# Performance work log

Measured on AMD Instinct MI355X. Metric: run time of the kernel, lower is better.

The kernel has to match this reference:

```python
import jax, jax.numpy as jnp
import numpy as np

HIDDEN = 512
HEADS = 8
HEAD_DIM = HIDDEN // HEADS
EPS_LN = 1e-5
EPS_ATTN = 1e-6


def setup_inputs() -> dict:
    key = jax.random.key(0)
    ks = jax.random.split(key, 12)
    B, S, N, D = 4, 12, 2048, HIDDEN
    s = 1.0 / np.sqrt(D)
    x = jax.random.normal(ks[0], (B, S, N, D), dtype=jnp.float32)
    Wq = jax.random.normal(ks[1], (D, D), dtype=jnp.float32) * s
    bq = jnp.zeros((D,), dtype=jnp.float32)
    Wk = jax.random.normal(ks[2], (D, D), dtype=jnp.float32) * s
    bk = jnp.zeros((D,), dtype=jnp.float32)
    Wv = jax.random.normal(ks[3], (D, D), dtype=jnp.float32) * s
    bv = jnp.zeros((D,), dtype=jnp.float32)
    Wo = jax.random.normal(ks[4], (D, D), dtype=jnp.float32) * s
    bo = jnp.zeros((D,), dtype=jnp.float32)
    ln_g = jnp.ones((D,), dtype=jnp.float32)
    ln_b = jnp.zeros((D,), dtype=jnp.float32)
    return {"x": x, "Wq": Wq, "bq": bq, "Wk": Wk, "bk": bk,
            "Wv": Wv, "bv": bv, "Wo": Wo, "bo": bo,
            "ln_g": ln_g, "ln_b": ln_b}


def _layer_norm(x, g, b):
    mu = jnp.mean(x, axis=-1, keepdims=True)
    var = jnp.var(x, axis=-1, keepdims=True)
    return (x - mu) * jax.lax.rsqrt(var + EPS_LN) * g + b


def reference(x, Wq, bq, Wk, bk, Wv, bv, Wo, bo, ln_g, ln_b):
    B, S, N, D = x.shape
    L = S * N  # flattened spatiotemporal tokens
    residual = x
    h = _layer_norm(x, ln_g, ln_b).reshape(B, L, D)
    # projections; [B, L, D] -> [B, H, L, hd]
    def split_heads(t):
        return t.reshape(B, L, HEADS, HEAD_DIM).transpose(0, 2, 1, 3)
    q = split_heads(h @ Wq.T + bq)
    k = split_heads(h @ Wk.T + bk)
    v = split_heads(h @ Wv.T + bv)
    # elu+1 feature map
    q = jax.nn.elu(q) + 1.0
    k = jax.nn.elu(k) + 1.0
    # kv outer product: [B, H, hd, hd]
    kv = jnp.einsum('bhld,bhle->bhde', k, v)
    out = jnp.einsum('bhld,bhde->bhle', q, kv)
    normalizer = jnp.einsum('bhld,bhd->bhl', q, k.sum(axis=2))
    out = out / (normalizer[..., None] + EPS_ATTN)
    out = out.transpose(0, 2, 1, 3).reshape(B, L, D)
    out = out @ Wo.T + bo
    out = out.reshape(B, S, N, D)
    return out + residual
```

## Files before the change

### kernel.cpp

```cpp
#include <hip/hip_runtime.h>
#include <hip/hip_bf16.h>
#include <stdint.h>

#define DDIM 512
#define NHEAD 8
#define BATCH 4
#define LTOK 24576
#define MROWS 98304
#define MBLK 768
#define MBLK_B 192
#define PTILE 4160

typedef __attribute__((ext_vector_type(8))) short short8;
typedef __attribute__((ext_vector_type(4))) float f32x4;

__device__ __forceinline__ float bf2f(unsigned short u) {
  union { unsigned int i; float f; } c; c.i = ((unsigned int)u) << 16; return c.f;
}
__device__ __forceinline__ unsigned short f2bf(float f) {
  union { float f; unsigned int i; } c; c.f = f;
  unsigned int r = c.i + 0x7FFFu + ((c.i >> 16) & 1u);
  return (unsigned short)(r >> 16);
}
__device__ __forceinline__ void gload16(const void* g, void* l) {
  __builtin_amdgcn_global_load_lds((const __attribute__((address_space(1))) void*)g,
                                   (__attribute__((address_space(3))) void*)l, 16, 0, 0);
}
__device__ __forceinline__ float elu1(float v) { return (v > 0.f) ? (v + 1.f) : __expf(v); }

__global__ __launch_bounds__(256) void wprep(const float* __restrict__ Wq, const float* __restrict__ bq,
                                             const float* __restrict__ Wk, const float* __restrict__ bk,
                                             const float* __restrict__ Wv, const float* __restrict__ bv,
                                             const float* __restrict__ Wo,
                                             unsigned short* __restrict__ wf,
                                             unsigned short* __restrict__ wob,
                                             float* __restrict__ biasf) {
  long t = (long)blockIdx.x * 256 + threadIdx.x;
  if (t < 786432) {
    int f = (int)(t >> 9), c = (int)(t & 511);
    const float* src;
    if (f < 1024) { int hh = f >> 7, kv = (f >> 6) & 1, d = f & 63;
                    src = (kv ? Wv : Wk) + (long)(hh * 64 + d) * 512; }
    else          src = Wq + (long)(f - 1024) * 512;
    wf[t] = f2bf(src[c]);
  } else if (t < 786432 + 262144) {
    long i = t - 786432; wob[i] = f2bf(Wo[i]);
  } else if (t < 786432 + 262144 + 1536) {
    int f = (int)(t - (786432 + 262144));
    float v;
    if (f < 1024) { int hh = f >> 7, kv = (f >> 6) & 1, d = f & 63; v = (kv ? bv : bk)[hh * 64 + d]; }
    else v = bq[f - 1024];
    biasf[f] = v;
  }
}

__global__ __launch_bounds__(256) void ln_kernel(const float* __restrict__ x,
                                                 const float* __restrict__ g,
                                                 const float* __restrict__ b,
                                                 unsigned short* __restrict__ h) {
  int wv = threadIdx.x >> 6, lane = threadIdx.x & 63;
  long row = (long)blockIdx.x * 4 + wv;
  const float* xr = x + row * DDIM + lane * 8;
  float4 v0 = *(const float4*)xr;
  float4 v1 = *(const float4*)(xr + 4);
  float s  = v0.x + v0.y + v0.z + v0.w + v1.x + v1.y + v1.z + v1.w;
  float s2 = v0.x*v0.x + v0.y*v0.y + v0.z*v0.z + v0.w*v0.w
           + v1.x*v1.x + v1.y*v1.y + v1.z*v1.z + v1.w*v1.w;
  #pragma unroll
  for (int o = 32; o; o >>= 1) { s += __shfl_xor(s, o); s2 += __shfl_xor(s2, o); }
  float mu = s * (1.0f / DDIM);
  float var = s2 * (1.0f / DDIM) - mu * mu;
  float rs = rsqrtf(var + 1e-5f);
  float4 g0 = *(const float4*)(g + lane * 8);
  float4 g1 = *(const float4*)(g + lane * 8 + 4);
  float4 b0 = *(const float4*)(b + lane * 8);
  float4 b1 = *(const float4*)(b + lane * 8 + 4);
  short8 o;
  o[0] = (short)f2bf((v0.x - mu) * rs * g0.x + b0.x);
  o[1] = (short)f2bf((v0.y - mu) * rs * g0.y + b0.y);
  o[2] = (short)f2bf((v0.z - mu) * rs * g0.z + b0.z);
  o[3] = (short)f2bf((v0.w - mu) * rs * g0.w + b0.w);
  o[4] = (short)f2bf((v1.x - mu) * rs * g1.x + b1.x);
  o[5] = (short)f2bf((v1.y - mu) * rs * g1.y + b1.y);
  o[6] = (short)f2bf((v1.z - mu) * rs * g1.z + b1.z);
  o[7] = (short)f2bf((v1.w - mu) * rs * g1.w + b1.w);
  *(short8*)(h + row * DDIM + lane * 8) = o;
}

__global__ __launch_bounds__(256) void qkv_gemm(const unsigned short* __restrict__ A,
                                                const unsigned short* __restrict__ wf,
                                                const float* __restrict__ biasf,
                                                unsigned short* __restrict__ qbuf,
                                                unsigned short* __restrict__ part) {
  __shared__ union {
    struct { unsigned short As[128 * 64]; unsigned short Bs[128 * 64]; } st;
    struct { unsigned short kT[64 * 136]; unsigned short vT[64 * 136]; } tr;
    unsigned short Cs[128 * 136];
  } sm;

  int t = threadIdx.x;
  int wv = t >> 6, lane = t & 63;
  int wm = wv >> 1, wn = wv & 1;
  int kg = lane >> 4, lr = lane & 15;

  int lin = blockIdx.x;
  int g = lin / 96, r = lin % 96;
  int xb = g * 8 + (r & 7);
  int y  = r >> 3;
  long mBase = (long)xb * 128;
  int nBase = y * 128;

  f32x4 acc[4][4];
  #pragma unroll
  for (int m = 0; m < 4; m++)
    #pragma unroll
    for (int n = 0; n < 4; n++) acc[m][n] = (f32x4){0.f, 0.f, 0.f, 0.f};

  const unsigned short* Ab = A + mBase * DDIM;
  const unsigned short* Wb = wf + (long)nBase * DDIM;

  for (int k0 = 0; k0 < DDIM; k0 += 64) {
    #pragma unroll
    for (int i = 0; i < 4; i++) {
      int c = i * 256 + t;
      int rr = c >> 3, cc = c & 7;
      int sc = ((cc ^ (rr & 7)) << 3);
      gload16(Ab + (long)rr * DDIM + k0 + sc, sm.st.As + c * 8);
      gload16(Wb + (long)rr * DDIM + k0 + sc, sm.st.Bs + c * 8);
    }
    __syncthreads();
    #pragma unroll
    for (int kk = 0; kk < 2; kk++) {
      short8 a[4], b[4];
      #pragma unroll
      for (int m = 0; m < 4; m++) {
        int row = wm * 64 + m * 16 + lr;
        a[m] = *(const short8*)&sm.st.As[row * 64 + (((kk * 4 + kg) ^ (row & 7)) << 3)];
      }
      #pragma unroll
      for (int n = 0; n < 4; n++) {
        int row = wn * 64 + n * 16 + lr;
        b[n] = *(const short8*)&sm.st.Bs[row * 64 + (((kk * 4 + kg) ^ (row & 7)) << 3)];
      }
      #pragma unroll
      for (int m = 0; m < 4; m++)
        #pragma unroll
        for (int n = 0; n < 4; n++)
          acc[m][n] = __builtin_amdgcn_mfma_f32_16x16x32_bf16(a[m], b[n], acc[m][n], 0, 0, 0);
    }
    __syncthreads();
  }

  if (y < 8) {
    #pragma unroll
    for (int n = 0; n < 4; n++) {
      int col = wn * 64 + n * 16 + lr;
      float bv = biasf[nBase + col];
      #pragma unroll
      for (int m = 0; m < 4; m++)
        #pragma unroll
        for (int j = 0; j < 4; j++) {
          int row = wm * 64 + m * 16 + kg * 4 + j;
          float v = acc[m][n][j] + bv;
          if (wn == 0) sm.tr.kT[col * 136 + row] = f2bf(elu1(v));
          else         sm.tr.vT[(col - 64) * 136 + row] = f2bf(v);
        }
    }
    __syncthreads();
    f32x4 pacc[4];
    #pragma unroll
    for (int n = 0; n < 4; n++) pacc[n] = (f32x4){0.f, 0.f, 0.f, 0.f};
    short8 a[4];
    #pragma unroll
    for (int kk = 0; kk < 4; kk++)
      a[kk] = *(const short8*)&sm.tr.kT[(wv * 16 + lr) * 136 + kk * 32 + kg * 8];
    #pragma unroll
    for (int n = 0; n < 4; n++)
      #pragma unroll
      for (int kk = 0; kk < 4; kk++) {
        short8 b = *(const short8*)&sm.tr.vT[(n * 16 + lr) * 136 + kk * 32 + kg * 8];
        pacc[n] = __builtin_amdgcn_mfma_f32_16x16x32_bf16(a[kk], b, pacc[n], 0, 0, 0);
      }
    int batch = (int)(mBase / LTOK);
    int cIdx = xb % MBLK_B;
    long pbase = ((long)(batch * 8 + y) * MBLK_B + cIdx) * PTILE;
    #pragma unroll
    for (int n = 0; n < 4; n++)
      #pragma unroll
      for (int j = 0; j < 4; j++) {
        int d = wv * 16 + kg * 4 + j, e = n * 16 + lr;
        part[pbase + d * 64 + e] = f2bf(pacc[n][j]);
      }
    if (t < 64) {
      float s = 0.f;
      #pragma unroll
      for (int p = 0; p < 16; p++) {
        short8 kk8 = *(const short8*)&sm.tr.kT[t * 136 + p * 8];
        #pragma unroll
        for (int q = 0; q < 8; q++) s += bf2f((unsigned short)kk8[q]);
      }
      part[pbase + 4096 + t] = f2bf(s);
    }
  } else {
    #pragma unroll
    for (int n = 0; n < 4; n++) {
      int col = wn * 64 + n * 16 + lr;
      float bv = biasf[nBase + col];
      #pragma unroll
      for (int m = 0; m < 4; m++)
        #pragma unroll
        for (int j = 0; j < 4; j++) {
          int row = wm * 64 + m * 16 + kg * 4 + j;
          sm.Cs[row * 136 + col] = f2bf(elu1(acc[m][n][j] + bv));
        }
    }
    __syncthreads();
    int nq = y - 8;
    #pragma unroll
    for (int p = 0; p < 8; p++) {
      int idx = p * 256 + t;
      int row = idx >> 4, c8 = idx & 15;
      *(short8*)&qbuf[(mBase + row) * DDIM + nq * 128 + c8 * 8] =
          *(const short8*)&sm.Cs[row * 136 + c8 * 8];
    }
  }
}

__global__ __launch_bounds__(256) void kv_final(const unsigned short* __restrict__ part,
                                                unsigned short* __restrict__ kvD,
                                                float* __restrict__ ksum) {
  int bh = blockIdx.x;
  int idx = blockIdx.y * 256 + threadIdx.x;
  if (idx >= PTILE) return;
  const unsigned short* base = part + (long)bh * MBLK_B * PTILE + idx;
  float s = 0.f;
  for (int c = 0; c < MBLK_B; c++) s += bf2f(base[(long)c * PTILE]);
  if (idx < 4096) kvD[bh * 4096 + idx] = f2bf(s);
  else            ksum[bh * 64 + (idx - 4096)] = s;
}

__global__ __launch_bounds__(512) void w2_gemm(const unsigned short* __restrict__ kvD,
                                               const unsigned short* __restrict__ wob,
                                               unsigned short* __restrict__ Bmat) {
  __shared__ unsigned short W2s[512 * 72];
  int t = threadIdx.x, wv = t >> 6, lane = t & 63;
  int kg = lane >> 4, lr = lane & 15;
  int bh = blockIdx.x, b = bh >> 3, h = bh & 7;
  const unsigned short* kva = kvD + bh * 4096;

  short8 a[4][2];
  #pragma unroll
  for (int m = 0; m < 4; m++)
    #pragma unroll
    for (int kk = 0; kk < 2; kk++)
      a[m][kk] = *(const short8*)&kva[(m * 16 + lr) * 64 + kk * 32 + kg * 8];

  f32x4 acc[4][4];
  #pragma unroll
  for (int m = 0; m < 4; m++)
    #pragma unroll
    for (int n = 0; n < 4; n++) acc[m][n] = (f32x4){0.f, 0.f, 0.f, 0.f};

  #pragma unroll
  for (int n = 0; n < 4; n++) {
    int c = wv * 64 + n * 16 + lr;
    #pragma unroll
    for (int kk = 0; kk < 2; kk++) {
      short8 bfr = *(const short8*)&wob[(long)c * 512 + h * 64 + kk * 32 + kg * 8];
      #pragma unroll
      for (int m = 0; m < 4; m++)
        acc[m][n] = __builtin_amdgcn_mfma_f32_16x16x32_bf16(a[m][kk], bfr, acc[m][n], 0, 0, 0);
    }
  }
  #pragma unroll
  for (int m = 0; m < 4; m++)
    #pragma unroll
    for (int n = 0; n < 4; n++)
      #pragma unroll
      for (int j = 0; j < 4; j++)
        W2s[(wv * 64 + n * 16 + lr) * 72 + m * 16 + kg * 4 + j] = f2bf(acc[m][n][j]);
  __syncthreads();
  #pragma unroll
  for (int pp = 0; pp < 8; pp++) {
    int idx = pp * 512 + t;
    int c = idx >> 3, ch = (idx & 7) * 8;
    *(short8*)&Bmat[(long)b * 262144 + (long)c * 512 + h * 64 + ch] =
        *(const short8*)&W2s[c * 72 + ch];
  }
}

__global__ __launch_bounds__(256) void qscale(unsigned short* __restrict__ q,
                                              const float* __restrict__ ksum) {
  int wv = threadIdx.x >> 6, lane = threadIdx.x & 63;
  long row = (long)blockIdx.x * 4 + wv;
  int batch = (int)(row / LTOK);
  int bh = batch * 8 + (lane >> 3);
  unsigned short* qr = q + row * DDIM + lane * 8;
  short8 qv = *(const short8*)qr;
  const float* ks = ksum + bh * 64 + (lane & 7) * 8;
  float4 k0 = *(const float4*)ks;
  float4 k1 = *(const float4*)(ks + 4);
  float qf[8];
  #pragma unroll
  for (int j = 0; j < 8; j++) qf[j] = bf2f((unsigned short)qv[j]);
  float n = qf[0]*k0.x + qf[1]*k0.y + qf[2]*k0.z + qf[3]*k0.w
          + qf[4]*k1.x + qf[5]*k1.y + qf[6]*k1.z + qf[7]*k1.w;
  n += __shfl_xor(n, 1);
  n += __shfl_xor(n, 2);
  n += __shfl_xor(n, 4);
  float s = 1.0f / (n + 1e-6f);
  short8 o;
  #pragma unroll
  for (int j = 0; j < 8; j++) o[j] = (short)f2bf(qf[j] * s);
  *(short8*)qr = o;
}

__global__ __launch_bounds__(256) void ogemm(const unsigned short* __restrict__ A,
                                             const unsigned short* __restrict__ Bm,
                                             const float* __restrict__ bo,
                                             const float* __restrict__ xres,
                                             float* __restrict__ out) {
  __shared__ union {
    struct { unsigned short As[128 * 64]; unsigned short Bs[128 * 64]; } st;
    float Cs[64 * 132];
  } sm;

  int t = threadIdx.x;
  int wv = t >> 6, lane = t & 63;
  int wm = wv >> 1, wn = wv & 1;
  int kg = lane >> 4, lr = lane & 15;

  int lin = blockIdx.x;
  int g = lin >> 5, r = lin & 31;
  int xb = g * 8 + (r & 7);
  int y  = r >> 3;
  long mBase = (long)xb * 128;
  int nBase = y * 128;
  int batch = xb / MBLK_B;

  f32x4 acc[4][4];
  #pragma unroll
  for (int m = 0; m < 4; m++)
    #pragma unroll
    for (int n = 0; n < 4; n++) acc[m][n] = (f32x4){0.f, 0.f, 0.f, 0.f};

  const unsigned short* Ab = A + mBase * DDIM;
  const unsigned short* Bb = Bm + (long)batch * 262144 + (long)nBase * DDIM;

  for (int k0 = 0; k0 < DDIM; k0 += 64) {
    #pragma unroll
    for (int i = 0; i < 4; i++) {
      int c = i * 256 + t;
      int rr = c >> 3, cc = c & 7;
      int sc = ((cc ^ (rr & 7)) << 3);
      gload16(Ab + (long)rr * DDIM + k0 + sc, sm.st.As + c * 8);
      gload16(Bb + (long)rr * DDIM + k0 + sc, sm.st.Bs + c * 8);
    }
    __syncthreads();
    #pragma unroll
    for (int kk = 0; kk < 2; kk++) {
      short8 a[4], b[4];
      #pragma unroll
      for (int m = 0; m < 4; m++) {
        int row = wm * 64 + m * 16 + lr;
        a[m] = *(const short8*)&sm.st.As[row * 64 + (((kk * 4 + kg) ^ (row & 7)) << 3)];
      }
      #pragma unroll
      for (int n = 0; n < 4; n++) {
        int row = wn * 64 + n * 16 + lr;
        b[n] = *(const short8*)&sm.st.Bs[row * 64 + (((kk * 4 + kg) ^ (row & 7)) << 3)];
      }
      #pragma unroll
      for (int m = 0; m < 4; m++)
        #pragma unroll
        for (int n = 0; n < 4; n++)
          acc[m][n] = __builtin_amdgcn_mfma_f32_16x16x32_bf16(a[m], b[n], acc[m][n], 0, 0, 0);
    }
    __syncthreads();
  }

  for (int p = 0; p < 2; p++) {
    __syncthreads();
    if (wm == p) {
      #pragma unroll
      for (int n = 0; n < 4; n++) {
        int col = wn * 64 + n * 16 + lr;
        float bv = bo[nBase + col];
        #pragma unroll
        for (int m = 0; m < 4; m++)
          #pragma unroll
          for (int j = 0; j < 4; j++) {
            int lrow = m * 16 + kg * 4 + j;
            sm.Cs[lrow * 132 + col] = acc[m][n][j] + bv;
          }
      }
    }
    __syncthreads();
    #pragma unroll
    for (int pp = 0; pp < 8; pp++) {
      int idx = pp * 256 + t;
      int row = idx >> 5, c4 = idx & 31;
      long goff = (mBase + p * 64 + row) * DDIM + nBase + c4 * 4;
      float4 rv = *(const float4*)&xres[goff];
      float4 cv = *(const float4*)&sm.Cs[row * 132 + c4 * 4];
      float4 ov; ov.x = cv.x + rv.x; ov.y = cv.y + rv.y; ov.z = cv.z + rv.z; ov.w = cv.w + rv.w;
      *(float4*)&out[goff] = ov;
    }
  }
}

extern "C" void kernel_launch(void* const* d_in, const int* in_sizes, int n_in,
                              void* d_out, int out_size, void* d_ws, size_t ws_size,
                              hipStream_t stream) {
  const float* x    = (const float*)d_in[0];
  const float* Wq   = (const float*)d_in[1];
  const float* bq   = (const float*)d_in[2];
  const float* Wk   = (const float*)d_in[3];
  const float* bk   = (const float*)d_in[4];
  const float* Wv   = (const float*)d_in[5];
  const float* bv   = (const float*)d_in[6];
  const float* Wo   = (const float*)d_in[7];
  const float* bo   = (const float*)d_in[8];
  const float* ln_g = (const float*)d_in[9];
  const float* ln_b = (const float*)d_in[10];

  char* ws = (char*)d_ws;
  size_t SZ = (size_t)MROWS * DDIM * 2;
  unsigned short* hbuf = (unsigned short*)ws;
  unsigned short* qbuf = (unsigned short*)(ws + SZ);
  char* p = ws + 2 * SZ;
  unsigned short* wf   = (unsigned short*)p;  p += (size_t)1536 * 512 * 2;
  unsigned short* wob  = (unsigned short*)p;  p += (size_t)512 * 512 * 2;
  float* biasf         = (float*)p;           p += 1536 * 4;
  p = (char*)(((uintptr_t)p + 255) & ~(uintptr_t)255);
  unsigned short* part = (unsigned short*)p;  p += (size_t)6144 * PTILE * 2;
  unsigned short* kvD  = (unsigned short*)p;  p += (size_t)32 * 4096 * 2;
  float* ksum          = (float*)p;           p += 32 * 64 * 4;
  p = (char*)(((uintptr_t)p + 255) & ~(uintptr_t)255);
  unsigned short* Bmat = (unsigned short*)p;  p += (size_t)BATCH * 512 * 512 * 2;

  wprep<<<(786432 + 262144 + 1536 + 255) / 256, 256, 0, stream>>>(Wq, bq, Wk, bk, Wv, bv, Wo,
                                                                  wf, wob, biasf);
  ln_kernel<<<MROWS / 4, 256, 0, stream>>>(x, ln_g, ln_b, hbuf);
  qkv_gemm<<<MBLK * 12, 256, 0, stream>>>(hbuf, wf, biasf, qbuf, part);
  kv_final<<<dim3(32, (PTILE + 255) / 256), 256, 0, stream>>>(part, kvD, ksum);
  w2_gemm<<<32, 512, 0, stream>>>(kvD, wob, Bmat);
  qscale<<<MROWS / 4, 256, 0, stream>>>(qbuf, ksum);
  ogemm<<<MBLK * 4, 256, 0, stream>>>(qbuf, Bmat, bo, x, (float*)d_out);
}
```

Measured before the change: 511.4 us.

## Rewrite QKV GEMM with 256x256 tiles and a double-buffered pipelined K loop

The QKV projection GEMM moves from 128x128 tiles with 256 threads to 256x256 tiles with 512 threads. The K loop is restructured into half-tile stages over a 128KB LDS double buffer, with explicit vmcnt waits, s_setprio and sched barriers so global-to-LDS loads overlap the MFMA work. The KV partial epilogue now handles two heads per block and gets the key sum from an MFMA against a ones row, which halves the partial buffer and the kv_final reduction depth. The cost is higher register and LDS pressure, much larger unrolled code, and hand-counted waitcnt values that must stay correct.

```diff
diff --git a/kernel.cpp b/kernel.cpp
--- a/kernel.cpp
+++ b/kernel.cpp
@@ -7,8 +7,10 @@
 #define BATCH 4
 #define LTOK 24576
 #define MROWS 98304
-#define MBLK 768
-#define MBLK_B 192
+#define QKV_MBLK 384
+#define KVCH 96
+#define OG_MBLK 768
+#define OG_MBLK_B 192
 #define PTILE 4160
 
 typedef __attribute__((ext_vector_type(8))) short short8;
@@ -87,141 +89,251 @@
   *(short8*)(h + row * DDIM + lane * 8) = o;
 }
 
-__global__ __launch_bounds__(256) void qkv_gemm(const unsigned short* __restrict__ A,
-                                                const unsigned short* __restrict__ wf,
-                                                const float* __restrict__ biasf,
-                                                unsigned short* __restrict__ qbuf,
-                                                unsigned short* __restrict__ part) {
-  __shared__ union {
-    struct { unsigned short As[128 * 64]; unsigned short Bs[128 * 64]; } st;
-    struct { unsigned short kT[64 * 136]; unsigned short vT[64 * 136]; } tr;
-    unsigned short Cs[128 * 136];
-  } sm;
-
-  int t = threadIdx.x;
-  int wv = t >> 6, lane = t & 63;
-  int wm = wv >> 1, wn = wv & 1;
+
+__device__ __forceinline__ short8 ldsfrag(const unsigned short* h, int row, int kg) {
+  return *(const short8*)&h[row * 32 + ((kg ^ ((row >> 1) & 3)) << 3)];
+}
+
+__device__ __forceinline__ void stage_half(const unsigned short* gbase,
+                                           unsigned short* ldsbase, int tid) {
+  #pragma unroll
+  for (int i = 0; i < 2; i++) {
+    int c = i * 512 + tid;
+    int rr = c >> 2, cc = c & 3;
+    int sc = ((cc ^ ((rr >> 1) & 3)) << 3);
+    gload16(gbase + (long)rr * DDIM + sc, ldsbase + c * 8);
+  }
+}
+
+template <int VMP1, int VMP3, bool S01, bool S23>
+__device__ __forceinline__ void ktile(int t, unsigned short* lds,
+                                      const unsigned short* Ab, const unsigned short* Wb,
+                                      f32x4 (&acc)[8][4],
+                                      int wm, int wn, int lr, int kg, int tid) {
+  const int buf = t & 1;
+  unsigned short* A0l = lds + (buf * 2 + 0) * 8192;
+  unsigned short* A1l = lds + (buf * 2 + 1) * 8192;
+  unsigned short* B0l = lds + 32768 + (buf * 2 + 0) * 8192;
+  unsigned short* B1l = lds + 32768 + (buf * 2 + 1) * 8192;
+  unsigned short* A1n = lds + ((buf ^ 1) * 2 + 1) * 8192;
+  unsigned short* B1n = lds + 32768 + ((buf ^ 1) * 2 + 1) * 8192;
+  short8 a[4], b[4];
+
+  #pragma unroll
+  for (int m = 0; m < 4; m++) a[m] = ldsfrag(A0l, wm * 128 + m * 16 + lr, kg);
+  #pragma unroll
+  for (int n = 0; n < 4; n++) b[n] = ldsfrag(B0l, wn * 64 + n * 16 + lr, kg);
+  if (S01) stage_half(Ab + (long)(t + 1) * 64 + 32, A1n, tid);
+  __builtin_amdgcn_s_barrier();
+  __builtin_amdgcn_s_setprio(1);
+  #pragma unroll
+  for (int m = 0; m < 4; m++)
+    #pragma unroll
+    for (int n = 0; n < 4; n++)
+      acc[m][n] = __builtin_amdgcn_mfma_f32_16x16x32_bf16(a[m], b[n], acc[m][n], 0, 0, 0);
+  __builtin_amdgcn_s_setprio(0);
+  __builtin_amdgcn_s_barrier();
+  __builtin_amdgcn_sched_barrier(0);
+
+  #pragma unroll
+  for (int m = 0; m < 4; m++) a[m] = ldsfrag(A0l, wm * 128 + (4 + m) * 16 + lr, kg);
+  if (S01) stage_half(Wb + (long)(t + 1) * 64 + 32, B1n, tid);
+  __builtin_amdgcn_s_barrier();
+  __builtin_amdgcn_s_setprio(1);
+  #pragma unroll
+  for (int m = 0; m < 4; m++)
+    #pragma unroll
+    for (int n = 0; n < 4; n++)
+      acc[4 + m][n] = __builtin_amdgcn_mfma_f32_16x16x32_bf16(a[m], b[n], acc[4 + m][n], 0, 0, 0);
+  __builtin_amdgcn_s_setprio(0);
+  asm volatile("s_waitcnt vmcnt(%0)" :: "i"(VMP1) : "memory");
+  __builtin_amdgcn_s_barrier();
+  __builtin_amdgcn_sched_barrier(0);
+
+  #pragma unroll
+  for (int m = 0; m < 4; m++) a[m] = ldsfrag(A1l, wm * 128 + m * 16 + lr, kg);
+  #pragma unroll
+  for (int n = 0; n < 4; n++) b[n] = ldsfrag(B1l, wn * 64 + n * 16 + lr, kg);
+  if (S23) stage_half(Ab + (long)(t + 2) * 64, A0l, tid);
+  __builtin_amdgcn_s_barrier();
+  __builtin_amdgcn_s_setprio(1);
+  #pragma unroll
+  for (int m = 0; m < 4; m++)
+    #pragma unroll
+    for (int n = 0; n < 4; n++)
+      acc[m][n] = __builtin_amdgcn_mfma_f32_16x16x32_bf16(a[m], b[n], acc[m][n], 0, 0, 0);
+  __builtin_amdgcn_s_setprio(0);
+  __builtin_amdgcn_s_barrier();
+  __builtin_amdgcn_sched_barrier(0);
+
+  #pragma unroll
+  for (int m = 0; m < 4; m++) a[m] = ldsfrag(A1l, wm * 128 + (4 + m) * 16 + lr, kg);
+  if (S23) stage_half(Wb + (long)(t + 2) * 64, B0l, tid);
+  __builtin_amdgcn_s_barrier();
+  __builtin_amdgcn_s_setprio(1);
+  #pragma unroll
+  for (int m = 0; m < 4; m++)
+    #pragma unroll
+    for (int n = 0; n < 4; n++)
+      acc[4 + m][n] = __builtin_amdgcn_mfma_f32_16x16x32_bf16(a[m], b[n], acc[4 + m][n], 0, 0, 0);
+  __builtin_amdgcn_s_setprio(0);
+  asm volatile("s_waitcnt vmcnt(%0)" :: "i"(VMP3) : "memory");
+  __builtin_amdgcn_s_barrier();
+  __builtin_amdgcn_sched_barrier(0);
+}
+
+__global__ __launch_bounds__(512, 2) void qkv_gemm(const unsigned short* __restrict__ A,
+                                                   const unsigned short* __restrict__ wf,
+                                                   const float* __restrict__ biasf,
+                                                   unsigned short* __restrict__ qbuf,
+                                                   unsigned short* __restrict__ part) {
+  __shared__ unsigned short lds[65536];
+
+  int tid = threadIdx.x;
+  int wv = tid >> 6, lane = tid & 63;
+  int wm = wv >> 2, wn = wv & 3;
   int kg = lane >> 4, lr = lane & 15;
 
   int lin = blockIdx.x;
-  int g = lin / 96, r = lin % 96;
+  int g = lin / 48, r = lin % 48;
   int xb = g * 8 + (r & 7);
   int y  = r >> 3;
-  long mBase = (long)xb * 128;
-  int nBase = y * 128;
-
-  f32x4 acc[4][4];
-  #pragma unroll
-  for (int m = 0; m < 4; m++)
-    #pragma unroll
-    for (int n = 0; n < 4; n++) acc[m][n] = (f32x4){0.f, 0.f, 0.f, 0.f};
+  long mBase = (long)xb * 256;
+  int nBase = y * 256;
 
   const unsigned short* Ab = A + mBase * DDIM;
   const unsigned short* Wb = wf + (long)nBase * DDIM;
 
-  for (int k0 = 0; k0 < DDIM; k0 += 64) {
-    #pragma unroll
-    for (int i = 0; i < 4; i++) {
-      int c = i * 256 + t;
-      int rr = c >> 3, cc = c & 7;
-      int sc = ((cc ^ (rr & 7)) << 3);
-      gload16(Ab + (long)rr * DDIM + k0 + sc, sm.st.As + c * 8);
-      gload16(Wb + (long)rr * DDIM + k0 + sc, sm.st.Bs + c * 8);
-    }
-    __syncthreads();
-    #pragma unroll
-    for (int kk = 0; kk < 2; kk++) {
-      short8 a[4], b[4];
-      #pragma unroll
-      for (int m = 0; m < 4; m++) {
-        int row = wm * 64 + m * 16 + lr;
-        a[m] = *(const short8*)&sm.st.As[row * 64 + (((kk * 4 + kg) ^ (row & 7)) << 3)];
-      }
-      #pragma unroll
-      for (int n = 0; n < 4; n++) {
-        int row = wn * 64 + n * 16 + lr;
-        b[n] = *(const short8*)&sm.st.Bs[row * 64 + (((kk * 4 + kg) ^ (row & 7)) << 3)];
-      }
-      #pragma unroll
-      for (int m = 0; m < 4; m++)
-        #pragma unroll
-        for (int n = 0; n < 4; n++)
-          acc[m][n] = __builtin_amdgcn_mfma_f32_16x16x32_bf16(a[m], b[n], acc[m][n], 0, 0, 0);
-    }
-    __syncthreads();
-  }
-
-  if (y < 8) {
-    #pragma unroll
-    for (int n = 0; n < 4; n++) {
-      int col = wn * 64 + n * 16 + lr;
-      float bv = biasf[nBase + col];
-      #pragma unroll
-      for (int m = 0; m < 4; m++)
+  f32x4 acc[8][4];
+  #pragma unroll
+  for (int m = 0; m < 8; m++)
+    #pragma unroll
+    for (int n = 0; n < 4; n++) acc[m][n] = (f32x4){0.f, 0.f, 0.f, 0.f};
+
+  stage_half(Ab,       lds + 0 * 8192, tid);
+  stage_half(Wb,       lds + 32768 + 0 * 8192, tid);
+  stage_half(Ab + 32,  lds + 1 * 8192, tid);
+  stage_half(Wb + 32,  lds + 32768 + 1 * 8192, tid);
+  stage_half(Ab + 64,  lds + 2 * 8192, tid);
+  stage_half(Wb + 64,  lds + 32768 + 2 * 8192, tid);
+  asm volatile("s_waitcnt vmcnt(8)" ::: "memory");
+  __builtin_amdgcn_s_barrier();
+  __builtin_amdgcn_sched_barrier(0);
+
+  #pragma unroll 1
+  for (int i = 0; i < 3; i++) {
+    ktile<8, 8, true, true>(2 * i,     lds, Ab, Wb, acc, wm, wn, lr, kg, tid);
+    ktile<8, 8, true, true>(2 * i + 1, lds, Ab, Wb, acc, wm, wn, lr, kg, tid);
+  }
+  ktile<8, 4, true, false>(6, lds, Ab, Wb, acc, wm, wn, lr, kg, tid);
+  ktile<0, 63, false, false>(7, lds, Ab, Wb, acc, wm, wn, lr, kg, tid);
+
+  __syncthreads();
+
+  if (y < 4) {
+    unsigned short* kT = lds;
+    unsigned short* vT = lds + 16896;
+    int batch = xb / KVCH;
+    int cIdx  = xb % KVCH;
+
+    {
+      int rr = 64 + (tid >> 5), cc = tid & 31;
+      short8 z;
+      #pragma unroll
+      for (int j = 0; j < 8; j++) z[j] = (rr == 64) ? (short)0x3F80 : (short)0;
+      *(short8*)&vT[rr * 264 + cc * 8] = z;
+    }
+
+    #pragma unroll 1
+    for (int p = 0; p < 2; p++) {
+      if ((wn >> 1) == p) {
+        bool isV = wn & 1;
+        #pragma unroll
+        for (int n = 0; n < 4; n++) {
+          int feat = n * 16 + lr;
+          float bv = biasf[nBase + wn * 64 + n * 16 + lr];
+          #pragma unroll
+          for (int m = 0; m < 8; m++)
+            #pragma unroll
+            for (int j = 0; j < 4; j++) {
+              int tok = wm * 128 + m * 16 + kg * 4 + j;
+              float v = acc[m][n][j] + bv;
+              if (!isV) kT[feat * 264 + tok] = f2bf(elu1(v));
+              else      vT[feat * 264 + tok] = f2bf(v);
+            }
+        }
+      }
+      __syncthreads();
+
+      int mt = wv & 3, ngrp = wv >> 2;
+      int h = y * 2 + p;
+      long pbase = ((long)(batch * 8 + h) * KVCH + cIdx) * PTILE;
+      if (!ngrp) {
+        f32x4 pa0 = {0,0,0,0}, pa1 = {0,0,0,0}, pa2 = {0,0,0,0};
+        #pragma unroll
+        for (int kk = 0; kk < 8; kk++) {
+          short8 af = *(const short8*)&kT[(mt * 16 + lr) * 264 + kk * 32 + kg * 8];
+          short8 b0 = *(const short8*)&vT[(0 * 16 + lr) * 264 + kk * 32 + kg * 8];
+          short8 b1 = *(const short8*)&vT[(1 * 16 + lr) * 264 + kk * 32 + kg * 8];
+          short8 b2 = *(const short8*)&vT[(2 * 16 + lr) * 264 + kk * 32 + kg * 8];
+          pa0 = __builtin_amdgcn_mfma_f32_16x16x32_bf16(af, b0, pa0, 0, 0, 0);
+          pa1 = __builtin_amdgcn_mfma_f32_16x16x32_bf16(af, b1, pa1, 0, 0, 0);
+          pa2 = __builtin_amdgcn_mfma_f32_16x16x32_bf16(af, b2, pa2, 0, 0, 0);
+        }
         #pragma unroll
         for (int j = 0; j < 4; j++) {
-          int row = wm * 64 + m * 16 + kg * 4 + j;
-          float v = acc[m][n][j] + bv;
-          if (wn == 0) sm.tr.kT[col * 136 + row] = f2bf(elu1(v));
-          else         sm.tr.vT[(col - 64) * 136 + row] = f2bf(v);
+          int d = mt * 16 + kg * 4 + j;
+          part[pbase + d * 64 + (0 * 16 + lr)] = f2bf(pa0[j]);
+          part[pbase + d * 64 + (1 * 16 + lr)] = f2bf(pa1[j]);
+          part[pbase + d * 64 + (2 * 16 + lr)] = f2bf(pa2[j]);
         }
-    }
-    __syncthreads();
-    f32x4 pacc[4];
-    #pragma unroll
-    for (int n = 0; n < 4; n++) pacc[n] = (f32x4){0.f, 0.f, 0.f, 0.f};
-    short8 a[4];
-    #pragma unroll
-    for (int kk = 0; kk < 4; kk++)
-      a[kk] = *(const short8*)&sm.tr.kT[(wv * 16 + lr) * 136 + kk * 32 + kg * 8];
-    #pragma unroll
-    for (int n = 0; n < 4; n++)
-      #pragma unroll
-      for (int kk = 0; kk < 4; kk++) {
-        short8 b = *(const short8*)&sm.tr.vT[(n * 16 + lr) * 136 + kk * 32 + kg * 8];
-        pacc[n] = __builtin_amdgcn_mfma_f32_16x16x32_bf16(a[kk], b, pacc[n], 0, 0, 0);
-      }
-    int batch = (int)(mBase / LTOK);
-    int cIdx = xb % MBLK_B;
-    long pbase = ((long)(batch * 8 + y) * MBLK_B + cIdx) * PTILE;
-    #pragma unroll
-    for (int n = 0; n < 4; n++)
-      #pragma unroll
-      for (int j = 0; j < 4; j++) {
-        int d = wv * 16 + kg * 4 + j, e = n * 16 + lr;
-        part[pbase + d * 64 + e] = f2bf(pacc[n][j]);
-      }
-    if (t < 64) {
-      float s = 0.f;
-      #pragma unroll
-      for (int p = 0; p < 16; p++) {
-        short8 kk8 = *(const short8*)&sm.tr.kT[t * 136 + p * 8];
-        #pragma unroll
-        for (int q = 0; q < 8; q++) s += bf2f((unsigned short)kk8[q]);
-      }
-      part[pbase + 4096 + t] = f2bf(s);
+      } else {
+        f32x4 pa0 = {0,0,0,0}, pa1 = {0,0,0,0};
+        #pragma unroll
+        for (int kk = 0; kk < 8; kk++) {
+          short8 af = *(const short8*)&kT[(mt * 16 + lr) * 264 + kk * 32 + kg * 8];
+          short8 b0 = *(const short8*)&vT[(3 * 16 + lr) * 264 + kk * 32 + kg * 8];
+          short8 b1 = *(const short8*)&vT[(4 * 16 + lr) * 264 + kk * 32 + kg * 8];
+          pa0 = __builtin_amdgcn_mfma_f32_16x16x32_bf16(af, b0, pa0, 0, 0, 0);
+          pa1 = __builtin_amdgcn_mfma_f32_16x16x32_bf16(af, b1, pa1, 0, 0, 0);
+        }
+        #pragma unroll
+        for (int j = 0; j < 4; j++) {
+          int d = mt * 16 + kg * 4 + j;
+          part[pbase + d * 64 + (3 * 16 + lr)] = f2bf(pa0[j]);
+          if (lr == 0) part[pbase + 4096 + d] = f2bf(pa1[j]);
+        }
+      }
+      __syncthreads();
     }
   } else {
-    #pragma unroll
-    for (int n = 0; n < 4; n++) {
-      int col = wn * 64 + n * 16 + lr;
-      float bv = biasf[nBase + col];
-      #pragma unroll
-      for (int m = 0; m < 4; m++)
-        #pragma unroll
-        for (int j = 0; j < 4; j++) {
-          int row = wm * 64 + m * 16 + kg * 4 + j;
-          sm.Cs[row * 136 + col] = f2bf(elu1(acc[m][n][j] + bv));
+    unsigned short* Cs = lds;
+    int qc0 = (y - 4) * 256;
+    #pragma unroll 1
+    for (int half = 0; half < 2; half++) {
+      if (wm == half) {
+        #pragma unroll
+        for (int n = 0; n < 4; n++) {
+          int col = wn * 64 + n * 16 + lr;
+          float bv = biasf[nBase + col];
+          #pragma unroll
+          for (int m = 0; m < 8; m++)
+            #pragma unroll
+            for (int j = 0; j < 4; j++) {
+              int rowl = m * 16 + kg * 4 + j;
+              Cs[rowl * 264 + col] = f2bf(elu1(acc[m][n][j] + bv));
+            }
         }
-    }
-    __syncthreads();
-    int nq = y - 8;
-    #pragma unroll
-    for (int p = 0; p < 8; p++) {
-      int idx = p * 256 + t;
-      int row = idx >> 4, c8 = idx & 15;
-      *(short8*)&qbuf[(mBase + row) * DDIM + nq * 128 + c8 * 8] =
-          *(const short8*)&sm.Cs[row * 136 + c8 * 8];
+      }
+      __syncthreads();
+      #pragma unroll
+      for (int i = 0; i < 8; i++) {
+        int idx = i * 512 + tid;
+        int row = idx >> 5, ch = idx & 31;
+        *(short8*)&qbuf[(mBase + half * 128 + row) * DDIM + qc0 + ch * 8] =
+            *(const short8*)&Cs[row * 264 + ch * 8];
+      }
+      __syncthreads();
     }
   }
 }
@@ -232,9 +344,9 @@
   int bh = blockIdx.x;
   int idx = blockIdx.y * 256 + threadIdx.x;
   if (idx >= PTILE) return;
-  const unsigned short* base = part + (long)bh * MBLK_B * PTILE + idx;
+  const unsigned short* base = part + (long)bh * KVCH * PTILE + idx;
   float s = 0.f;
-  for (int c = 0; c < MBLK_B; c++) s += bf2f(base[(long)c * PTILE]);
+  for (int c = 0; c < KVCH; c++) s += bf2f(base[(long)c * PTILE]);
   if (idx < 4096) kvD[bh * 4096 + idx] = f2bf(s);
   else            ksum[bh * 64 + (idx - 4096)] = s;
 }
@@ -336,7 +448,7 @@
   int y  = r >> 3;
   long mBase = (long)xb * 128;
   int nBase = y * 128;
-  int batch = xb / MBLK_B;
+  int batch = xb / OG_MBLK_B;
 
   f32x4 acc[4][4];
   #pragma unroll
@@ -433,7 +545,7 @@
   unsigned short* wob  = (unsigned short*)p;  p += (size_t)512 * 512 * 2;
   float* biasf         = (float*)p;           p += 1536 * 4;
   p = (char*)(((uintptr_t)p + 255) & ~(uintptr_t)255);
-  unsigned short* part = (unsigned short*)p;  p += (size_t)6144 * PTILE * 2;
+  unsigned short* part = (unsigned short*)p;  p += (size_t)32 * KVCH * PTILE * 2;
   unsigned short* kvD  = (unsigned short*)p;  p += (size_t)32 * 4096 * 2;
   float* ksum          = (float*)p;           p += 32 * 64 * 4;
   p = (char*)(((uintptr_t)p + 255) & ~(uintptr_t)255);
@@ -442,9 +554,9 @@
   wprep<<<(786432 + 262144 + 1536 + 255) / 256, 256, 0, stream>>>(Wq, bq, Wk, bk, Wv, bv, Wo,
                                                                   wf, wob, biasf);
   ln_kernel<<<MROWS / 4, 256, 0, stream>>>(x, ln_g, ln_b, hbuf);
-  qkv_gemm<<<MBLK * 12, 256, 0, stream>>>(hbuf, wf, biasf, qbuf, part);
+  qkv_gemm<<<QKV_MBLK * 6, 512, 0, stream>>>(hbuf, wf, biasf, qbuf, part);
   kv_final<<<dim3(32, (PTILE + 255) / 256), 256, 0, stream>>>(part, kvD, ksum);
   w2_gemm<<<32, 512, 0, stream>>>(kvD, wob, Bmat);
   qscale<<<MROWS / 4, 256, 0, stream>>>(qbuf, ksum);
-  ogemm<<<MBLK * 4, 256, 0, stream>>>(qbuf, Bmat, bo, x, (float*)d_out);
-}
+  ogemm<<<OG_MBLK * 4, 256, 0, stream>>>(qbuf, Bmat, bo, x, (float*)d_out);
+}
```

Result: no change. 515.3 us (+0.8%).
